# Kernel tuning notes

Hardware: AMD Instinct MI355X
Metric: run time of the kernel (lower is better)

The kernel has to match this reference:

```python
import jax, jax.numpy as jnp
import numpy as np

WS = 7        # window size
SHIFT = 3     # shift size (ws // 2)
NH = 8        # num heads
EPS = 1e-5


def _ln(x, g, b):
    m = x.mean(-1, keepdims=True)
    v = ((x - m) ** 2).mean(-1, keepdims=True)
    return (x - m) / jnp.sqrt(v + EPS) * g + b


def setup_inputs() -> dict:
    key = jax.random.key(0)
    B, Hh, Ww, C = 8, 112, 112, 256
    N = Hh * Ww
    hidden = 4 * C
    ks = jax.random.split(key, 12)
    x = jax.random.normal(ks[0], (B, N, C), jnp.float32)

    # --- standard Swin shifted-window additive attention mask ---
    img_mask = np.zeros((Hh, Ww), np.float32)
    cnt = 0
    for hs in (slice(0, -WS), slice(-WS, -SHIFT), slice(-SHIFT, None)):
        for wsl in (slice(0, -WS), slice(-WS, -SHIFT), slice(-SHIFT, None)):
            img_mask[hs, wsl] = cnt
            cnt += 1
    mw = img_mask.reshape(Hh // WS, WS, Ww // WS, WS).transpose(0, 2, 1, 3).reshape(-1, WS * WS)
    am = mw[:, None, :] - mw[:, :, None]
    mask_matrix = jnp.asarray(np.where(am != 0, -100.0, 0.0).astype(np.float32))  # (nW, 49, 49)

    s = 0.02
    return dict(
        x=x,
        mask_matrix=mask_matrix,
        norm1_g=jnp.ones((C,), jnp.float32),
        norm1_b=jnp.zeros((C,), jnp.float32),
        qkv_w=jax.random.normal(ks[1], (C, 3 * C), jnp.float32) * s,
        qkv_b=jnp.zeros((3 * C,), jnp.float32),
        proj_w=jax.random.normal(ks[2], (C, C), jnp.float32) * s,
        proj_b=jnp.zeros((C,), jnp.float32),
        norm2_g=jnp.ones((C,), jnp.float32),
        norm2_b=jnp.zeros((C,), jnp.float32),
        fc1_w=jax.random.normal(ks[3], (C, hidden), jnp.float32) * s,
        fc1_b=jnp.zeros((hidden,), jnp.float32),
        fc2_w=jax.random.normal(ks[4], (hidden, C), jnp.float32) * s,
        fc2_b=jnp.zeros((C,), jnp.float32),
        H=112,
        W=112,
    )


def reference(x, mask_matrix, norm1_g, norm1_b, qkv_w, qkv_b, proj_w, proj_b,
              norm2_g, norm2_b, fc1_w, fc1_b, fc2_w, fc2_b, H, W):
    B, N, C = x.shape
    hd = C // NH
    scale = hd ** (-0.5)
    wsws = WS * WS

    # --- SwinLocallyGroupedAttn on norm1(x) ---
    xa = _ln(x, norm1_g, norm1_b).reshape(B, H, W, C)
    pad_r = (WS - W % WS) % WS
    pad_b = (WS - H % WS) % WS
    if pad_r > 0 or pad_b > 0:
        xa = jnp.pad(xa, ((0, 0), (0, pad_b), (0, pad_r), (0, 0)))
    Hp, Wp = H + pad_b, W + pad_r
    xa = jnp.roll(xa, shift=(-SHIFT, -SHIFT), axis=(1, 2))
    h_, w_ = Hp // WS, Wp // WS
    nW = h_ * w_
    # window partition: (B*nW, ws*ws, C)
    xw = xa.reshape(B, h_, WS, w_, WS, C).transpose(0, 1, 3, 2, 4, 5).reshape(B * nW, wsws, C)
    qkv = (xw @ qkv_w + qkv_b).reshape(B * nW, wsws, 3, NH, hd).transpose(2, 0, 3, 1, 4)
    q, k, v = qkv[0], qkv[1], qkv[2]          # (B*nW, NH, wsws, hd)
    attn = jnp.einsum('wnqd,wnkd->wnqk', q, k) * scale
    attn = attn.reshape(B, nW, NH, wsws, wsws) + mask_matrix[None, :, None]
    attn = jax.nn.softmax(attn, axis=-1).reshape(B * nW, NH, wsws, wsws)
    out = jnp.einsum('wnqk,wnkd->wnqd', attn, v).transpose(0, 2, 1, 3).reshape(B * nW, wsws, C)
    out = out @ proj_w + proj_b
    # window reverse + un-shift + crop
    out = out.reshape(B, h_, w_, WS, WS, C).transpose(0, 1, 3, 2, 4, 5).reshape(B, Hp, Wp, C)
    out = jnp.roll(out, shift=(SHIFT, SHIFT), axis=(1, 2))
    out = out[:, :H, :W, :].reshape(B, N, C)
    x = x + out

    # --- MLP branch ---
    h = _ln(x, norm2_g, norm2_b)
    h = jax.nn.gelu(h @ fc1_w + fc1_b, approximate=False)
    x = x + (h @ fc2_w + fc2_b)
    return x
```

## Files before the change

kernel.cpp:

```cpp
#include <hip/hip_runtime.h>
#include <hip/hip_bf16.h>
#include <cstdint>

#define WS_    7
#define SHIFT_ 3
#define NH_    8
#define HD_    32
#define C_     256
#define H_     112
#define W_     112
#define B_     8
#define WSQ    49
#define ROWS   100352
#define HIDDEN 1024

typedef __attribute__((ext_vector_type(8))) short short8;
typedef __attribute__((ext_vector_type(4))) float f32x4;

__device__ inline ushort f2bf(float f){
  uint32_t u = __float_as_uint(f);
  u += 0x7fffu + ((u >> 16) & 1u);
  return (ushort)(u >> 16);
}

__device__ inline int row2tok(int r){
  int w  = r / WSQ, p = r - w * WSQ;
  int b  = w >> 8, wi = w & 255;
  int wh = wi >> 4, ww = wi & 15;
  int i  = p / WS_, j = p - i * WS_;
  int h  = wh * WS_ + i + SHIFT_; if (h >= H_) h -= H_;
  int wc = ww * WS_ + j + SHIFT_; if (wc >= W_) wc -= W_;
  return b * (H_ * W_) + h * W_ + wc;
}

__global__ void transpose_cast(const float* __restrict__ in, ushort* __restrict__ out,
                               int K, int N){
  int idx = blockIdx.x * 256 + threadIdx.x;
  if (idx >= K * N) return;
  int k = idx / N, n = idx - k * N;
  out[(size_t)n * K + k] = f2bf(in[idx]);
}

template<bool GATHER>
__global__ __launch_bounds__(256) void ln_kernel(const float* __restrict__ x,
    const float* __restrict__ g, const float* __restrict__ b, ushort* __restrict__ out)
{
  int wave = threadIdx.x >> 6, lane = threadIdx.x & 63;
  int r = blockIdx.x * 4 + wave;
  int t = GATHER ? row2tok(r) : r;
  const float4 v = *(const float4*)(x + (size_t)t * C_ + lane * 4);
  float s  = v.x + v.y + v.z + v.w;
  float s2 = v.x * v.x + v.y * v.y + v.z * v.z + v.w * v.w;
  #pragma unroll
  for (int m = 32; m; m >>= 1){ s += __shfl_xor(s, m); s2 += __shfl_xor(s2, m); }
  float mean = s * (1.f / C_);
  float inv  = rsqrtf(fmaxf(s2 * (1.f / C_) - mean * mean, 0.f) + 1e-5f);
  int c0 = lane * 4;
  ushort4 o;
  o.x = f2bf((v.x - mean) * inv * g[c0 + 0] + b[c0 + 0]);
  o.y = f2bf((v.y - mean) * inv * g[c0 + 1] + b[c0 + 1]);
  o.z = f2bf((v.z - mean) * inv * g[c0 + 2] + b[c0 + 2]);
  o.w = f2bf((v.w - mean) * inv * g[c0 + 3] + b[c0 + 3]);
  *(ushort4*)(out + (size_t)r * C_ + c0) = o;
}

__device__ inline void gll16(const void* g, void* l){
  __builtin_amdgcn_global_load_lds(
      (__attribute__((address_space(1))) void*)g,
      (__attribute__((address_space(3))) void*)l, 16, 0, 0);
}

template<int EPI>
__global__ __launch_bounds__(512, 4) void gemmW(
    const ushort* __restrict__ A,
    const ushort* __restrict__ Bt,
    const float*  __restrict__ bias,
    void*         __restrict__ Cout,
    const float*  __restrict__ resid,
    int M, int N, int K, int nN)
{
  __shared__ __align__(16) ushort lA[2][128 * 32];
  __shared__ __align__(16) ushort lB[2][256 * 32];
  const int tid  = threadIdx.x;

  const int cpx  = gridDim.x >> 3;
  const int lid  = (blockIdx.x & 7) * cpx + (blockIdx.x >> 3);
  const int rowb = lid / nN, colb = lid - rowb * nN;
  const int m0   = rowb * 128, n0 = colb * 256;

  const int wave = tid >> 6, lane = tid & 63;
  const int wr   = wave >> 2, wc = wave & 3;
  const int la   = lane & 15, lg = lane >> 4;

  f32x4 acc[4][4] = {};

  const int r0 = tid >> 2, kp = (tid & 3) * 8;
  const ushort* gA  = A  + (size_t)(m0 + r0)       * K + kp;
  const ushort* gB0 = Bt + (size_t)(n0 + r0)       * K + kp;
  const ushort* gB1 = Bt + (size_t)(n0 + r0 + 128) * K + kp;

  const int nt = K >> 5;
  int buf = 0;

  gll16(gA,  &lA[0][tid * 8]);
  gll16(gB0, &lB[0][tid * 8]);
  gll16(gB1, &lB[0][(tid + 512) * 8]);
  __syncthreads();

  for (int t = 0; t < nt; ++t){
    if (t + 1 < nt){
      const int k0 = (t + 1) * 32;
      gll16(gA  + k0, &lA[buf ^ 1][tid * 8]);
      gll16(gB0 + k0, &lB[buf ^ 1][tid * 8]);
      gll16(gB1 + k0, &lB[buf ^ 1][(tid + 512) * 8]);
    }
    short8 af[4], bfr[4];
    #pragma unroll
    for (int i = 0; i < 4; i++) af[i]  = *(const short8*)&lA[buf][(wr * 64 + i * 16 + la) * 32 + lg * 8];
    #pragma unroll
    for (int j = 0; j < 4; j++) bfr[j] = *(const short8*)&lB[buf][(wc * 64 + j * 16 + la) * 32 + lg * 8];
    #pragma unroll
    for (int i = 0; i < 4; i++)
      #pragma unroll
      for (int j = 0; j < 4; j++)
        acc[i][j] = __builtin_amdgcn_mfma_f32_16x16x32_bf16(af[i], bfr[j], acc[i][j], 0, 0, 0);
    __syncthreads();
    buf ^= 1;
  }

  #pragma unroll
  for (int i = 0; i < 4; i++){
    #pragma unroll
    for (int j = 0; j < 4; j++){
      int col = n0 + wc * 64 + j * 16 + la;
      float bs = bias[col];
      #pragma unroll
      for (int q = 0; q < 4; q++){
        int row = m0 + wr * 64 + i * 16 + lg * 4 + q;
        float v = acc[i][j][q] + bs;
        if (EPI == 0){
          ((ushort*)Cout)[(size_t)row * N + col] = f2bf(v);
        } else if (EPI == 1){
          int t = row2tok(row);
          size_t o = (size_t)t * C_ + col;
          ((float*)Cout)[o] = resid[o] + v;
        } else if (EPI == 2){
          float gx = 0.5f * v * (1.f + erff(v * 0.70710678118f));
          ((ushort*)Cout)[(size_t)row * N + col] = f2bf(gx);
        } else {
          size_t o = (size_t)row * C_ + col;
          ((float*)Cout)[o] = resid[o] + v;
        }
      }
    }
  }
}

__global__ __launch_bounds__(256, 2) void attn_kernel(const ushort* __restrict__ qkv,
    const float* __restrict__ mask, ushort* __restrict__ out)
{
  __shared__ __align__(16) ushort P [4][64 * 72];
  __shared__ __align__(16) ushort VT[4][32 * 72];
  const int wave = threadIdx.x >> 6, lane = threadIdx.x & 63;
  const int gid  = blockIdx.x * 4 + wave;
  const int w    = gid >> 3, head = gid & 7;
  const int la   = lane & 15, lg = lane >> 4;
  const ushort* qb = qkv + (size_t)w * WSQ * 768 + head * HD_;
  const short8 z8 = {0,0,0,0,0,0,0,0};

  {
    ushort4 z4 = {0,0,0,0};
    for (int idx = lane; idx < (32 * 72) / 4; idx += 64) ((ushort4*)VT[wave])[idx] = z4;
    for (int idx = lane; idx < WSQ * 4; idx += 64){
      int row = idx >> 2, db = idx & 3;
      short8 vv = *(const short8*)&qb[(size_t)row * 768 + 512 + db * 8];
      #pragma unroll
      for (int e = 0; e < 8; e++) VT[wave][(db * 8 + e) * 72 + row] = ((ushort*)&vv)[e];
    }
  }

  short8 qf[4], kf[4];
  #pragma unroll
  for (int i = 0; i < 4; i++){
    int m = i * 16 + la;
    qf[i] = (m < WSQ) ? *(const short8*)&qb[(size_t)m * 768 +       lg * 8] : z8;
    kf[i] = (m < WSQ) ? *(const short8*)&qb[(size_t)m * 768 + 256 + lg * 8] : z8;
  }

  f32x4 s[4][4] = {};
  #pragma unroll
  for (int i = 0; i < 4; i++)
    #pragma unroll
    for (int j = 0; j < 4; j++)
      s[i][j] = __builtin_amdgcn_mfma_f32_16x16x32_bf16(qf[i], kf[j], s[i][j], 0, 0, 0);

  const float* mrow = mask + (size_t)(w & 255) * WSQ * WSQ;
  const float scale = 0.17677669529663687f;
  float rinv[4][4];
  #pragma unroll
  for (int i = 0; i < 4; i++){
    #pragma unroll
    for (int q = 0; q < 4; q++){
      int m = i * 16 + lg * 4 + q;
      float pv[4]; float mx = -1e30f;
      #pragma unroll
      for (int j = 0; j < 4; j++){
        int n = j * 16 + la;
        float val = (m < WSQ && n < WSQ) ? s[i][j][q] * scale + mrow[m * WSQ + n] : -1e30f;
        pv[j] = val; mx = fmaxf(mx, val);
      }
      #pragma unroll
      for (int msk = 1; msk < 16; msk <<= 1) mx = fmaxf(mx, __shfl_xor(mx, msk));
      float sum = 0.f;
      #pragma unroll
      for (int j = 0; j < 4; j++){ float e = __expf(pv[j] - mx); pv[j] = e; sum += e; }
      #pragma unroll
      for (int msk = 1; msk < 16; msk <<= 1) sum += __shfl_xor(sum, msk);
      rinv[i][q] = 1.f / sum;
      #pragma unroll
      for (int j = 0; j < 4; j++) P[wave][m * 72 + j * 16 + la] = f2bf(pv[j]);
    }
  }

  f32x4 o[4][2] = {};
  #pragma unroll
  for (int kk = 0; kk < 2; kk++){
    short8 pf[4], vf[2];
    #pragma unroll
    for (int i = 0; i < 4; i++)  pf[i]  = *(const short8*)&P [wave][(i  * 16 + la) * 72 + kk * 32 + lg * 8];
    #pragma unroll
    for (int jn = 0; jn < 2; jn++) vf[jn] = *(const short8*)&VT[wave][(jn * 16 + la) * 72 + kk * 32 + lg * 8];
    #pragma unroll
    for (int i = 0; i < 4; i++)
      #pragma unroll
      for (int jn = 0; jn < 2; jn++)
        o[i][jn] = __builtin_amdgcn_mfma_f32_16x16x32_bf16(pf[i], vf[jn], o[i][jn], 0, 0, 0);
  }

  ushort* ob = out + (size_t)w * WSQ * C_ + head * HD_;
  #pragma unroll
  for (int i = 0; i < 4; i++)
    #pragma unroll
    for (int jn = 0; jn < 2; jn++)
      #pragma unroll
      for (int q = 0; q < 4; q++){
        int m = i * 16 + lg * 4 + q;
        if (m < WSQ) ob[(size_t)m * C_ + jn * 16 + la] = f2bf(o[i][jn][q] * rinv[i][q]);
      }
}

extern "C" void kernel_launch(void* const* d_in, const int* in_sizes, int n_in,
                              void* d_out, int out_size, void* d_ws, size_t ws_size,
                              hipStream_t stream)
{
  const float* x      = (const float*)d_in[0];
  const float* mask   = (const float*)d_in[1];
  const float* n1g    = (const float*)d_in[2];
  const float* n1b    = (const float*)d_in[3];
  const float* qkv_w  = (const float*)d_in[4];
  const float* qkv_b  = (const float*)d_in[5];
  const float* proj_w = (const float*)d_in[6];
  const float* proj_b = (const float*)d_in[7];
  const float* n2g    = (const float*)d_in[8];
  const float* n2b    = (const float*)d_in[9];
  const float* fc1_w  = (const float*)d_in[10];
  const float* fc1_b  = (const float*)d_in[11];
  const float* fc2_w  = (const float*)d_in[12];
  const float* fc2_b  = (const float*)d_in[13];

  char* ws = (char*)d_ws;
  ushort* R1 = (ushort*)ws;
  ushort* R2 = (ushort*)(ws + 51380224);
  float*  x2 = (float*) (ws + 51380224 + 205520896);
  ushort* wqT = (ushort*)(ws + 51380224 + 205520896 + 102760448);
  ushort* wpT = wqT + 768 * 256;
  ushort* w1T = wpT + 256 * 256;
  ushort* w2T = w1T + 1024 * 256;

  transpose_cast<<<(256 * 768  + 255) / 256, 256, 0, stream>>>(qkv_w,  wqT, 256, 768);
  transpose_cast<<<(256 * 256  + 255) / 256, 256, 0, stream>>>(proj_w, wpT, 256, 256);
  transpose_cast<<<(256 * 1024 + 255) / 256, 256, 0, stream>>>(fc1_w,  w1T, 256, 1024);
  transpose_cast<<<(1024 * 256 + 255) / 256, 256, 0, stream>>>(fc2_w,  w2T, 1024, 256);

  ln_kernel<true><<<ROWS / 4, 256, 0, stream>>>(x, n1g, n1b, R1);
  gemmW<0><<<784 * 3, 512, 0, stream>>>(R1, wqT, qkv_b, R2, nullptr, ROWS, 768, 256, 3);
  attn_kernel<<<(2048 * 8) / 4, 256, 0, stream>>>(R2, mask, R1);
  gemmW<1><<<784 * 1, 512, 0, stream>>>(R1, wpT, proj_b, x2, x, ROWS, 256, 256, 1);
  ln_kernel<false><<<ROWS / 4, 256, 0, stream>>>(x2, n2g, n2b, R1);
  gemmW<2><<<784 * 4, 512, 0, stream>>>(R1, w1T, fc1_b, R2, nullptr, ROWS, 1024, 256, 4);
  gemmW<3><<<784 * 1, 512, 0, stream>>>(R2, w2T, fc2_b, d_out, x2, ROWS, 256, 1024, 1);
}
```

Baseline: 674.4 us.

## Rewrite GEMM with 256x256x64 tiles, XOR-swizzled LDS and staged prefetch

Replaces the 128x256x32 double-buffered GEMM with a 256x256 tile and K=64 step. Global-to-LDS loads are split into quarter-tile stages and interleaved with MFMA sub-blocks. LDS columns are XOR-swizzled to avoid bank conflicts, and s_setprio raises priority around the MFMA bursts. The aim is more operand reuse per loaded byte and better overlap of loads with compute. The cost is 128 KB of LDS and 128 accumulator registers per thread, which lowers occupancy to about one block per CU; the grid also halves, so there are fewer blocks to balance across CUs.

```diff
diff --git a/kernel.cpp b/kernel.cpp
--- a/kernel.cpp
+++ b/kernel.cpp
@@ -71,7 +71,7 @@
 }
 
 template<int EPI>
-__global__ __launch_bounds__(512, 4) void gemmW(
+__global__ __launch_bounds__(512, 2) void gemm8p(
     const ushort* __restrict__ A,
     const ushort* __restrict__ Bt,
     const float*  __restrict__ bias,
@@ -79,65 +79,100 @@
     const float*  __restrict__ resid,
     int M, int N, int K, int nN)
 {
-  __shared__ __align__(16) ushort lA[2][128 * 32];
-  __shared__ __align__(16) ushort lB[2][256 * 32];
+  __shared__ __align__(16) ushort sA[2][256 * 64];
+  __shared__ __align__(16) ushort sB[2][256 * 64];
   const int tid  = threadIdx.x;
+  const int wave = tid >> 6, lane = tid & 63;
+  const int wr   = wave >> 2, wc = wave & 3;
+  const int la   = lane & 15, lg = lane >> 4;
+  const int l8   = lane >> 3, l7 = lane & 7;
 
   const int cpx  = gridDim.x >> 3;
   const int lid  = (blockIdx.x & 7) * cpx + (blockIdx.x >> 3);
   const int rowb = lid / nN, colb = lid - rowb * nN;
-  const int m0   = rowb * 128, n0 = colb * 256;
-
-  const int wave = tid >> 6, lane = tid & 63;
-  const int wr   = wave >> 2, wc = wave & 3;
-  const int la   = lane & 15, lg = lane >> 4;
-
-  f32x4 acc[4][4] = {};
-
-  const int r0 = tid >> 2, kp = (tid & 3) * 8;
-  const ushort* gA  = A  + (size_t)(m0 + r0)       * K + kp;
-  const ushort* gB0 = Bt + (size_t)(n0 + r0)       * K + kp;
-  const ushort* gB1 = Bt + (size_t)(n0 + r0 + 128) * K + kp;
-
-  const int nt = K >> 5;
-  int buf = 0;
-
-  gll16(gA,  &lA[0][tid * 8]);
-  gll16(gB0, &lB[0][tid * 8]);
-  gll16(gB1, &lB[0][(tid + 512) * 8]);
-  __syncthreads();
-
-  for (int t = 0; t < nt; ++t){
-    if (t + 1 < nt){
-      const int k0 = (t + 1) * 32;
-      gll16(gA  + k0, &lA[buf ^ 1][tid * 8]);
-      gll16(gB0 + k0, &lB[buf ^ 1][tid * 8]);
-      gll16(gB1 + k0, &lB[buf ^ 1][(tid + 512) * 8]);
-    }
-    short8 af[4], bfr[4];
-    #pragma unroll
-    for (int i = 0; i < 4; i++) af[i]  = *(const short8*)&lA[buf][(wr * 64 + i * 16 + la) * 32 + lg * 8];
-    #pragma unroll
-    for (int j = 0; j < 4; j++) bfr[j] = *(const short8*)&lB[buf][(wc * 64 + j * 16 + la) * 32 + lg * 8];
-    #pragma unroll
-    for (int i = 0; i < 4; i++)
-      #pragma unroll
-      for (int j = 0; j < 4; j++)
-        acc[i][j] = __builtin_amdgcn_mfma_f32_16x16x32_bf16(af[i], bfr[j], acc[i][j], 0, 0, 0);
-    __syncthreads();
-    buf ^= 1;
-  }
-
-  #pragma unroll
-  for (int i = 0; i < 4; i++){
-    #pragma unroll
-    for (int j = 0; j < 4; j++){
-      int col = n0 + wc * 64 + j * 16 + la;
+  const int m0   = rowb * 256, n0 = colb * 256;
+
+  const int swe      = (l7 ^ l8) * 8;
+  const int arow_off = (wave < 4 ? wave * 8 : 128 + (wave - 4) * 8) + l8;
+  const int brow_off = wave * 8 + l8;
+  const ushort* gA = A  + (size_t)(m0 + arow_off) * K + swe;
+  const ushort* gB = Bt + (size_t)(n0 + brow_off) * K + swe;
+
+#define STAGE_A(b, q, k0) gll16(gA + (size_t)(q) * 32 * K + (k0), &sA[b][(arow_off + (q) * 32) * 64 + l7 * 8])
+#define STAGE_B(b, c, k0) gll16(gB + (size_t)(c) * 64 * K + (k0), &sB[b][(brow_off + (c) * 64) * 64 + l7 * 8])
+
+  const int arow_rd = wr * 128 + la;
+  const int brow_rd = wc * 64 + la;
+  const int col0    = lg * 8;
+  const int xorm    = l7 * 8;
+#define LDA(sAb, m, ks) (*(const short8*)&(sAb)[(arow_rd + (m) * 16) * 64 + ((((ks) * 32) + col0) ^ xorm)])
+#define LDB(sBb, n, ks) (*(const short8*)&(sBb)[(brow_rd + (n) * 16) * 64 + ((((ks) * 32) + col0) ^ xorm)])
+
+  f32x4 acc[8][4] = {};
+  const int nt = K >> 6;
+
+  STAGE_A(0, 0, 0); STAGE_B(0, 0, 0);
+  STAGE_A(0, 1, 0); STAGE_B(0, 1, 0);
+  STAGE_A(0, 2, 0); STAGE_B(0, 2, 0);
+  STAGE_A(0, 3, 0); STAGE_B(0, 3, 0);
+  STAGE_A(1, 0, 64); STAGE_B(1, 0, 64);
+  STAGE_A(1, 1, 64); STAGE_B(1, 1, 64);
+  STAGE_A(1, 2, 64); STAGE_B(1, 2, 64);
+
+#define TILE(TT, S1c, S2c, VMLIT) do {                                        \
+    const int b_ = (TT) & 1; const int kc_ = (TT) * 64;                        \
+    ushort* sAb = sA[b_]; ushort* sBb = sB[b_];                                \
+    const bool S1_ = (S1c), S2_ = (S2c);                                       \
+      \
+    if (S1_){ STAGE_A(b_ ^ 1, 3, kc_ + 64); STAGE_B(b_ ^ 1, 3, kc_ + 64); }    \
+    asm volatile("s_waitcnt vmcnt(" VMLIT ")" ::: "memory");                   \
+    __builtin_amdgcn_s_barrier();                                              \
+    short8 bfr[4][2], af[2][2];                                                \
+    _Pragma("unroll") for (int n = 0; n < 4; n++)                              \
+      { _Pragma("unroll") for (int ks = 0; ks < 2; ks++) bfr[n][ks] = LDB(sBb, n, ks); } \
+    _Pragma("unroll") for (int mi = 0; mi < 2; mi++)                           \
+      { _Pragma("unroll") for (int ks = 0; ks < 2; ks++) af[mi][ks] = LDA(sAb, mi, ks); } \
+    __builtin_amdgcn_s_setprio(1);                                             \
+    _Pragma("unroll") for (int mi = 0; mi < 2; mi++)                           \
+      { _Pragma("unroll") for (int n = 0; n < 4; n++)                          \
+        { _Pragma("unroll") for (int ks = 0; ks < 2; ks++)                     \
+          acc[mi][n] = __builtin_amdgcn_mfma_f32_16x16x32_bf16(af[mi][ks], bfr[n][ks], acc[mi][n], 0, 0, 0); } } \
+    __builtin_amdgcn_s_setprio(0);                                             \
+    __builtin_amdgcn_s_barrier();                                              \
+     \
+    _Pragma("unroll") for (int q = 1; q < 4; q++){                             \
+      if (S2_){ STAGE_A(b_, q - 1, kc_ + 128); STAGE_B(b_, q - 1, kc_ + 128); } \
+      _Pragma("unroll") for (int mi = 0; mi < 2; mi++)                         \
+        { _Pragma("unroll") for (int ks = 0; ks < 2; ks++) af[mi][ks] = LDA(sAb, q * 2 + mi, ks); } \
+      __builtin_amdgcn_s_setprio(1);                                           \
+      _Pragma("unroll") for (int mi = 0; mi < 2; mi++)                         \
+        { _Pragma("unroll") for (int n = 0; n < 4; n++)                        \
+          { _Pragma("unroll") for (int ks = 0; ks < 2; ks++)                   \
+            acc[q * 2 + mi][n] = __builtin_amdgcn_mfma_f32_16x16x32_bf16(af[mi][ks], bfr[n][ks], acc[q * 2 + mi][n], 0, 0, 0); } } \
+      __builtin_amdgcn_s_setprio(0);                                           \
+      __builtin_amdgcn_s_barrier();                                            \
+    }                                                                          \
+  } while (0)
+
+  for (int t = 0; t < nt - 1; ++t) TILE(t, true, (t + 2) < nt, "8");
+  TILE(nt - 1, false, false, "0");
+
+#undef TILE
+#undef LDA
+#undef LDB
+#undef STAGE_A
+#undef STAGE_B
+
+  #pragma unroll
+  for (int m = 0; m < 8; m++){
+    #pragma unroll
+    for (int n = 0; n < 4; n++){
+      int col = n0 + wc * 64 + n * 16 + la;
       float bs = bias[col];
       #pragma unroll
       for (int q = 0; q < 4; q++){
-        int row = m0 + wr * 64 + i * 16 + lg * 4 + q;
-        float v = acc[i][j][q] + bs;
+        int row = m0 + wr * 128 + m * 16 + lg * 4 + q;
+        float v = acc[m][n][q] + bs;
         if (EPI == 0){
           ((ushort*)Cout)[(size_t)row * N + col] = f2bf(v);
         } else if (EPI == 1){
@@ -283,10 +318,10 @@
   transpose_cast<<<(1024 * 256 + 255) / 256, 256, 0, stream>>>(fc2_w,  w2T, 1024, 256);
 
   ln_kernel<true><<<ROWS / 4, 256, 0, stream>>>(x, n1g, n1b, R1);
-  gemmW<0><<<784 * 3, 512, 0, stream>>>(R1, wqT, qkv_b, R2, nullptr, ROWS, 768, 256, 3);
+  gemm8p<0><<<392 * 3, 512, 0, stream>>>(R1, wqT, qkv_b, R2, nullptr, ROWS, 768, 256, 3);
   attn_kernel<<<(2048 * 8) / 4, 256, 0, stream>>>(R2, mask, R1);
-  gemmW<1><<<784 * 1, 512, 0, stream>>>(R1, wpT, proj_b, x2, x, ROWS, 256, 256, 1);
+  gemm8p<1><<<392 * 1, 512, 0, stream>>>(R1, wpT, proj_b, x2, x, ROWS, 256, 256, 1);
   ln_kernel<false><<<ROWS / 4, 256, 0, stream>>>(x2, n2g, n2b, R1);
-  gemmW<2><<<784 * 4, 512, 0, stream>>>(R1, w1T, fc1_b, R2, nullptr, ROWS, 1024, 256, 4);
-  gemmW<3><<<784 * 1, 512, 0, stream>>>(R2, w2T, fc2_b, d_out, x2, ROWS, 256, 1024, 1);
-}
+  gemm8p<2><<<392 * 4, 512, 0, stream>>>(R1, w1T, fc1_b, R2, nullptr, ROWS, 1024, 256, 4);
+  gemm8p<3><<<392 * 1, 512, 0, stream>>>(R2, w2T, fc2_b, d_out, x2, ROWS, 256, 1024, 1);
+}
```

Result: slower. 918.4 us (+36.2%).

## Fuse LayerNorm2 into proj GEMM epilogue and triple-buffer GEMM K loop

Applied to the files above, without the earlier changes.

The second LayerNorm kernel is removed. The projection GEMM epilogue now adds the residual, writes x2 in window order, keeps a bf16 copy of the tile in LDS, and computes row statistics with shuffles plus an LDS reduction so it can emit the normalized bf16 activations directly. The fc2 epilogue then scatters back to token order using row2tok. Separately, the GEMM main loop moves to a 3-stage global_load_lds ring with explicit vmcnt waits and a single barrier per K step. The larger LDS footprint may cut blocks per CU, and the fused epilogue adds LDS traffic and barriers to the proj GEMM.

```diff
diff --git a/kernel.cpp b/kernel.cpp
--- a/kernel.cpp
+++ b/kernel.cpp
@@ -22,6 +22,7 @@
   u += 0x7fffu + ((u >> 16) & 1u);
   return (ushort)(u >> 16);
 }
+__device__ inline float bf2f(ushort s){ return __uint_as_float(((uint32_t)s) << 16); }
 
 __device__ inline int row2tok(int r){
   int w  = r / WSQ, p = r - w * WSQ;
@@ -41,13 +42,12 @@
   out[(size_t)n * K + k] = f2bf(in[idx]);
 }
 
-template<bool GATHER>
 __global__ __launch_bounds__(256) void ln_kernel(const float* __restrict__ x,
     const float* __restrict__ g, const float* __restrict__ b, ushort* __restrict__ out)
 {
   int wave = threadIdx.x >> 6, lane = threadIdx.x & 63;
   int r = blockIdx.x * 4 + wave;
-  int t = GATHER ? row2tok(r) : r;
+  int t = row2tok(r);
   const float4 v = *(const float4*)(x + (size_t)t * C_ + lane * 4);
   float s  = v.x + v.y + v.z + v.w;
   float s2 = v.x * v.x + v.y * v.y + v.z * v.z + v.w * v.w;
@@ -77,12 +77,18 @@
     const float*  __restrict__ bias,
     void*         __restrict__ Cout,
     const float*  __restrict__ resid,
+    const float*  __restrict__ g2,
+    const float*  __restrict__ b2,
+    ushort*       __restrict__ outLN,
     int M, int N, int K, int nN)
 {
-  __shared__ __align__(16) ushort lA[2][128 * 32];
-  __shared__ __align__(16) ushort lB[2][256 * 32];
+  union SMem {
+    struct { ushort lA[3][128 * 32]; ushort lB[3][256 * 32]; } g;
+    struct { ushort stile[128][256]; float red[128][4][2]; } e;
+  };
+  __shared__ __align__(16) SMem sm;
+
   const int tid  = threadIdx.x;
-
   const int cpx  = gridDim.x >> 3;
   const int lid  = (blockIdx.x & 7) * cpx + (blockIdx.x >> 3);
   const int rowb = lid / nN, colb = lid - rowb * nN;
@@ -100,56 +106,106 @@
   const ushort* gB1 = Bt + (size_t)(n0 + r0 + 128) * K + kp;
 
   const int nt = K >> 5;
-  int buf = 0;
-
-  gll16(gA,  &lA[0][tid * 8]);
-  gll16(gB0, &lB[0][tid * 8]);
-  gll16(gB1, &lB[0][(tid + 512) * 8]);
-  __syncthreads();
+
+  gll16(gA,       &sm.g.lA[0][tid * 8]);
+  gll16(gB0,      &sm.g.lB[0][tid * 8]);
+  gll16(gB1,      &sm.g.lB[0][(tid + 512) * 8]);
+  gll16(gA  + 32, &sm.g.lA[1][tid * 8]);
+  gll16(gB0 + 32, &sm.g.lB[1][tid * 8]);
+  gll16(gB1 + 32, &sm.g.lB[1][(tid + 512) * 8]);
 
   for (int t = 0; t < nt; ++t){
-    if (t + 1 < nt){
-      const int k0 = (t + 1) * 32;
-      gll16(gA  + k0, &lA[buf ^ 1][tid * 8]);
-      gll16(gB0 + k0, &lB[buf ^ 1][tid * 8]);
-      gll16(gB1 + k0, &lB[buf ^ 1][(tid + 512) * 8]);
-    }
+    if (t + 1 < nt) asm volatile("s_waitcnt vmcnt(3)" ::: "memory");
+    else            asm volatile("s_waitcnt vmcnt(0)" ::: "memory");
+    __builtin_amdgcn_s_barrier();
+
+    const int tn = t + 2;
+    if (tn < nt){
+      const int bn = tn % 3, k0 = tn * 32;
+      gll16(gA  + k0, &sm.g.lA[bn][tid * 8]);
+      gll16(gB0 + k0, &sm.g.lB[bn][tid * 8]);
+      gll16(gB1 + k0, &sm.g.lB[bn][(tid + 512) * 8]);
+    }
+
+    const int bc = t % 3;
+    const ushort* pA = sm.g.lA[bc];
+    const ushort* pB = sm.g.lB[bc];
     short8 af[4], bfr[4];
     #pragma unroll
-    for (int i = 0; i < 4; i++) af[i]  = *(const short8*)&lA[buf][(wr * 64 + i * 16 + la) * 32 + lg * 8];
-    #pragma unroll
-    for (int j = 0; j < 4; j++) bfr[j] = *(const short8*)&lB[buf][(wc * 64 + j * 16 + la) * 32 + lg * 8];
+    for (int i = 0; i < 4; i++) af[i]  = *(const short8*)&pA[(wr * 64 + i * 16 + la) * 32 + lg * 8];
+    #pragma unroll
+    for (int j = 0; j < 4; j++) bfr[j] = *(const short8*)&pB[(wc * 64 + j * 16 + la) * 32 + lg * 8];
     #pragma unroll
     for (int i = 0; i < 4; i++)
       #pragma unroll
       for (int j = 0; j < 4; j++)
         acc[i][j] = __builtin_amdgcn_mfma_f32_16x16x32_bf16(af[i], bfr[j], acc[i][j], 0, 0, 0);
+  }
+
+  if (EPI != 1){
+    #pragma unroll
+    for (int i = 0; i < 4; i++){
+      #pragma unroll
+      for (int j = 0; j < 4; j++){
+        int col = n0 + wc * 64 + j * 16 + la;
+        float bs = bias[col];
+        #pragma unroll
+        for (int q = 0; q < 4; q++){
+          int row = m0 + wr * 64 + i * 16 + lg * 4 + q;
+          float v = acc[i][j][q] + bs;
+          if (EPI == 0){
+            ((ushort*)Cout)[(size_t)row * N + col] = f2bf(v);
+          } else if (EPI == 2){
+            float gx = 0.5f * v * (1.f + erff(v * 0.70710678118f));
+            ((ushort*)Cout)[(size_t)row * N + col] = f2bf(gx);
+          } else {
+            int tk = row2tok(row);
+            ((float*)Cout)[(size_t)tk * C_ + col] = resid[(size_t)row * C_ + col] + v;
+          }
+        }
+      }
+    }
+  } else {
     __syncthreads();
-    buf ^= 1;
-  }
-
-  #pragma unroll
-  for (int i = 0; i < 4; i++){
-    #pragma unroll
-    for (int j = 0; j < 4; j++){
-      int col = n0 + wc * 64 + j * 16 + la;
-      float bs = bias[col];
+    #pragma unroll
+    for (int i = 0; i < 4; i++){
       #pragma unroll
       for (int q = 0; q < 4; q++){
-        int row = m0 + wr * 64 + i * 16 + lg * 4 + q;
-        float v = acc[i][j][q] + bs;
-        if (EPI == 0){
-          ((ushort*)Cout)[(size_t)row * N + col] = f2bf(v);
-        } else if (EPI == 1){
-          int t = row2tok(row);
-          size_t o = (size_t)t * C_ + col;
-          ((float*)Cout)[o] = resid[o] + v;
-        } else if (EPI == 2){
-          float gx = 0.5f * v * (1.f + erff(v * 0.70710678118f));
-          ((ushort*)Cout)[(size_t)row * N + col] = f2bf(gx);
-        } else {
-          size_t o = (size_t)row * C_ + col;
-          ((float*)Cout)[o] = resid[o] + v;
+        int rowL = wr * 64 + i * 16 + lg * 4 + q;
+        int tk   = row2tok(m0 + rowL);
+        float rs = 0.f, rs2 = 0.f;
+        #pragma unroll
+        for (int n = 0; n < 4; n++){
+          int colL = wc * 64 + n * 16 + la;
+          float v = acc[i][n][q] + bias[colL];
+          float s = resid[(size_t)tk * C_ + colL] + v;
+          ((float*)Cout)[(size_t)(m0 + rowL) * C_ + colL] = s;
+          sm.e.stile[rowL][colL] = f2bf(s);
+          rs += s; rs2 += s * s;
+        }
+        #pragma unroll
+        for (int msk = 1; msk < 16; msk <<= 1){
+          rs  += __shfl_xor(rs,  msk);
+          rs2 += __shfl_xor(rs2, msk);
+        }
+        if (la == 0){ sm.e.red[rowL][wc][0] = rs; sm.e.red[rowL][wc][1] = rs2; }
+      }
+    }
+    __syncthreads();
+    #pragma unroll
+    for (int i = 0; i < 4; i++){
+      #pragma unroll
+      for (int q = 0; q < 4; q++){
+        int rowL = wr * 64 + i * 16 + lg * 4 + q;
+        float s0 = sm.e.red[rowL][0][0] + sm.e.red[rowL][1][0] + sm.e.red[rowL][2][0] + sm.e.red[rowL][3][0];
+        float s1 = sm.e.red[rowL][0][1] + sm.e.red[rowL][1][1] + sm.e.red[rowL][2][1] + sm.e.red[rowL][3][1];
+        float mean = s0 * (1.f / C_);
+        float inv  = rsqrtf(fmaxf(s1 * (1.f / C_) - mean * mean, 0.f) + 1e-5f);
+        #pragma unroll
+        for (int n = 0; n < 4; n++){
+          int colL = wc * 64 + n * 16 + la;
+          float s = bf2f(sm.e.stile[rowL][colL]);
+          outLN[(size_t)(m0 + rowL) * C_ + colL] = f2bf((s - mean) * inv * g2[colL] + b2[colL]);
         }
       }
     }
@@ -282,11 +338,10 @@
   transpose_cast<<<(256 * 1024 + 255) / 256, 256, 0, stream>>>(fc1_w,  w1T, 256, 1024);
   transpose_cast<<<(1024 * 256 + 255) / 256, 256, 0, stream>>>(fc2_w,  w2T, 1024, 256);
 
-  ln_kernel<true><<<ROWS / 4, 256, 0, stream>>>(x, n1g, n1b, R1);
-  gemmW<0><<<784 * 3, 512, 0, stream>>>(R1, wqT, qkv_b, R2, nullptr, ROWS, 768, 256, 3);
+  ln_kernel<<<ROWS / 4, 256, 0, stream>>>(x, n1g, n1b, R1);
+  gemmW<0><<<784 * 3, 512, 0, stream>>>(R1, wqT, qkv_b, R2, nullptr, nullptr, nullptr, nullptr, ROWS, 768, 256, 3);
   attn_kernel<<<(2048 * 8) / 4, 256, 0, stream>>>(R2, mask, R1);
-  gemmW<1><<<784 * 1, 512, 0, stream>>>(R1, wpT, proj_b, x2, x, ROWS, 256, 256, 1);
-  ln_kernel<false><<<ROWS / 4, 256, 0, stream>>>(x2, n2g, n2b, R1);
-  gemmW<2><<<784 * 4, 512, 0, stream>>>(R1, w1T, fc1_b, R2, nullptr, ROWS, 1024, 256, 4);
-  gemmW<3><<<784 * 1, 512, 0, stream>>>(R2, w2T, fc2_b, d_out, x2, ROWS, 256, 1024, 1);
-}
+  gemmW<1><<<784 * 1, 512, 0, stream>>>(R1, wpT, proj_b, x2, x, n2g, n2b, R1, ROWS, 256, 256, 1);
+  gemmW<2><<<784 * 4, 512, 0, stream>>>(R1, w1T, fc1_b, R2, nullptr, nullptr, nullptr, nullptr, ROWS, 1024, 256, 4);
+  gemmW<3><<<784 * 1, 512, 0, stream>>>(R2, w2T, fc2_b, d_out, x2, nullptr, nullptr, nullptr, ROWS, 256, 1024, 1);
+}
```

Result: no change. 682.1 us (+1.1%).
